# Kernel optimization log

Hardware: AMD Instinct MI355X
Metric: run time of the kernel (lower is better)

## Reference

```python
import jax, jax.numpy as jnp
import numpy as np

E, H = 300, 256          # embedding_dim, GRU hidden per direction
D = 2 * H                # BiGRU output / GCN feature dim
V, PAD = 30000, 0
B, T_LEN, C_LEN = 128, 50, 200
N_GCN = 2
OUT = 3


def _gru_dir(x, Wih, Whh, bih, bhh):
    # x: [B,S,E] -> [B,S,H]; torch GRU equations
    h0 = jnp.zeros((x.shape[0], Whh.shape[1]), x.dtype)
    def step(h, xt):
        gi = xt @ Wih.T + bih                 # [B,3H]
        gh = h @ Whh.T + bhh
        ir, iz, inn = jnp.split(gi, 3, axis=-1)
        hr, hz, hn = jnp.split(gh, 3, axis=-1)
        r = jax.nn.sigmoid(ir + hr)
        z = jax.nn.sigmoid(iz + hz)
        n = jnp.tanh(inn + r * hn)
        hnew = (1.0 - z) * n + z * h
        return hnew, hnew
    _, hs = jax.lax.scan(step, h0, jnp.swapaxes(x, 0, 1))
    return jnp.swapaxes(hs, 0, 1)


def _bigru(x, wih, whh, bih, bhh):
    # wih:[2,3H,E] whh:[2,3H,H] bih/bhh:[2,3H]
    f = _gru_dir(x, wih[0], whh[0], bih[0], bhh[0])
    b = _gru_dir(x[:, ::-1], wih[1], whh[1], bih[1], bhh[1])[:, ::-1]
    return jnp.concatenate([f, b], axis=-1)   # [B,S,2H]


def _stance_attn(tgt_emb, clm_emb, gt, gc):
    tgt_ht = _bigru(tgt_emb, *gt)
    clm_ht = _bigru(clm_emb, *gc)
    tgt_last = tgt_ht[:, -1]
    # 'dot' attention: weight[b,c] = claim_ht[b,c] . target_last_ht[b]
    w = jnp.einsum('bcd,bd->bc', clm_ht, tgt_last)
    # NOTE: original `weight.masked_fill(mask==0, -1e9)` result is DISCARDED
    # (non-inplace torch op), so the mask has no effect -> faithfully omitted.
    return tgt_ht, clm_ht, jax.nn.softmax(w, axis=1)


def _gcn(tgt_ht, clm_ht, Ws):
    # StanceGCN: cat nodes, N_GCN layers of dot-correlation attention + residual relu
    node = jnp.concatenate([tgt_ht, clm_ht], axis=1)   # [B,N,D]
    T = tgt_ht.shape[1]
    for i in range(Ws.shape[0]):
        # dot correlation reduces to pairwise inner products (no [B,N,N,D] blowup);
        # `corr_score.masked_fill(adj==0,...)` is also discarded in the source.
        corr = jax.nn.softmax(jnp.einsum('bid,bjd->bij', node, node), axis=2)
        trans = jnp.einsum('bnd,ed->bne', node, Ws[i])  # Linear(bias=False)
        node = jax.nn.relu(node + jnp.einsum('bij,bjd->bid', corr, trans))
    return node[:, :T], node[:, T:]


def setup_inputs() -> dict:
    key = jax.random.key(0)
    ks = iter(jax.random.split(key, 64))
    def norm(shape, s=0.05):
        return (jax.random.normal(next(ks), shape, jnp.float32) * s)
    d = {}
    d['task_id'] = 0
    d['task_target'] = jax.random.randint(next(ks), (B, T_LEN), 0, V)
    d['shared_target'] = jax.random.randint(next(ks), (B, T_LEN), 0, V)
    d['task_claim'] = jax.random.randint(next(ks), (B, C_LEN), 0, V)
    d['shared_claim'] = jax.random.randint(next(ks), (B, C_LEN), 0, V)
    d['task_mask'] = jax.random.randint(next(ks), (B, C_LEN), 0, 2).astype(jnp.int32)
    d['shared_mask'] = jax.random.randint(next(ks), (B, C_LEN), 0, 2).astype(jnp.int32)
    N = T_LEN + C_LEN
    d['task_adj'] = jax.random.randint(next(ks), (B, N, N), 0, 2).astype(jnp.int32)
    d['shared_adj'] = jax.random.randint(next(ks), (B, N, N), 0, 2).astype(jnp.int32)
    d['emb'] = norm((V, E), 0.1).at[PAD].set(0.0)
    for g in ['tgt', 'tgc', 'sgt', 'sgc']:
        d[g + '_wih'] = norm((2, 3 * H, E))
        d[g + '_whh'] = norm((2, 3 * H, H))
        d[g + '_bih'] = norm((2, 3 * H))
        d[g + '_bhh'] = norm((2, 3 * H))
    d['gcn_task_W'] = norm((N_GCN, D, D))
    d['gcn_shared_W'] = norm((N_GCN, D, D))
    d['lin_W'] = norm((OUT, 2 * D))
    d['lin_b'] = norm((OUT,))
    return d


def reference(task_id, task_target, shared_target, task_claim, shared_claim,
              task_mask, shared_mask, task_adj, shared_adj,
              emb,
              tgt_wih, tgt_whh, tgt_bih, tgt_bhh,
              tgc_wih, tgc_whh, tgc_bih, tgc_bhh,
              sgt_wih, sgt_whh, sgt_bih, sgt_bhh,
              sgc_wih, sgc_whh, sgc_bih, sgc_bhh,
              gcn_task_W, gcn_shared_W, lin_W, lin_b):
    # embedding lookups (eval mode: all dropouts are identity)
    tt, tc = emb[task_target], emb[task_claim]
    st, sc = emb[shared_target], emb[shared_claim]
    t_tgt, t_clm, t_w = _stance_attn(tt, tc,
                                     (tgt_wih, tgt_whh, tgt_bih, tgt_bhh),
                                     (tgc_wih, tgc_whh, tgc_bih, tgc_bhh))
    s_tgt, s_clm, s_w = _stance_attn(st, sc,
                                     (sgt_wih, sgt_whh, sgt_bih, sgt_bhh),
                                     (sgc_wih, sgc_whh, sgc_bih, sgc_bhh))
    _, t_clm_rep = _gcn(t_tgt, t_clm, gcn_task_W)
    _, s_clm_rep = _gcn(s_tgt, s_clm, gcn_shared_W)
    # StanceLinear: attention-weighted claim pooling, concat, final linear
    task_rep = jnp.einsum('bc,bcd->bd', t_w, t_clm_rep)
    shared_rep = jnp.einsum('bc,bcd->bd', s_w, s_clm_rep)
    final = jnp.concatenate([task_rep, shared_rep], axis=1)   # [B, 4H+4H]
    return final @ lin_W.T + lin_b                            # [B, 3]
```

## Files before the change

kernel.cpp:

```cpp
#include <hip/hip_runtime.h>
#include <hip/hip_bf16.h>

namespace {

constexpr int B_  = 128;
constexpr int TL  = 50, CL = 200, NNODE = 250;
constexpr int H_  = 256, D_ = 512;
constexpr long NODE_ELE = 128L * 250 * 512;

typedef __attribute__((ext_vector_type(8))) short bf16x8;
typedef __attribute__((ext_vector_type(4))) float f32x4;

__device__ inline float bits2f(unsigned v) { union { unsigned u; float f; } c; c.u = v; return c.f; }
__device__ inline unsigned f2bits(float x) { union { float f; unsigned u; } c; c.f = x; return c.u; }
__device__ inline unsigned short bfbits(float x) {
  __hip_bfloat16 b = __float2bfloat16(x);
  return *(unsigned short*)&b;
}
__device__ inline float bfsel(uint2 v, int r) {
  unsigned w = (r < 2) ? v.x : v.y;
  return bits2f((r & 1) ? (w & 0xFFFF0000u) : (w << 16));
}
__device__ inline float sigf(float x)  { return 1.f / (1.f + __expf(-x)); }
__device__ inline float tanhf_(float x){ return 1.f - 2.f / (__expf(2.f * x) + 1.f); }

struct BGemmArgs {
  const __hip_bfloat16* A; const __hip_bfloat16* B;
  const int* idx; const float* bias; const __hip_bfloat16* Res;
  void* C;
  long aStride, bStride, biasStride, cStride, rStride;
  int M, N, Kreal, lda, ldb, ldc, zShiftA;
};

template<bool GATHER, int OUT>
__global__ __launch_bounds__(256) void bgemm_k(BGemmArgs g) {
  __shared__ __align__(16) char As[2][16384];
  __shared__ __align__(16) char Bs[2][16384];
  const int z = blockIdx.z;
  const int m0 = blockIdx.x * 128, n0 = blockIdx.y * 128;
  const int tid = threadIdx.x;
  const int lane = tid & 63, wv = tid >> 6;
  const int wr = wv >> 1, wc = wv & 1;
  const __hip_bfloat16* Ab = GATHER ? g.A : g.A + (long)(z >> g.zShiftA) * g.aStride;
  const __hip_bfloat16* Bb = g.B + (long)z * g.bStride;

  long asrc[4], bsrc[4];
  int ldso[4];
  #pragma unroll
  for (int c2 = 0; c2 < 4; ++c2) {
    int o = c2 * 256 + tid;
    int row = o >> 3, ko = o & 7;
    int colel = 8 * (ko ^ (row & 7));
    long arow = GATHER ? (long)g.idx[m0 + row] * g.lda : (long)(m0 + row) * g.lda;
    asrc[c2] = arow + colel;
    bsrc[c2] = (long)(n0 + row) * g.ldb + colel;
    ldso[c2] = o * 16;
  }

  f32x4 acc[4][4];
  #pragma unroll
  for (int i = 0; i < 4; ++i)
    #pragma unroll
    for (int j = 0; j < 4; ++j) acc[i][j] = (f32x4){0.f, 0.f, 0.f, 0.f};

  const int KT = g.Kreal >> 6;
  #pragma unroll
  for (int c2 = 0; c2 < 4; ++c2) {
    __builtin_amdgcn_global_load_lds(
        (const __attribute__((address_space(1))) unsigned*)(Ab + asrc[c2]),
        (__attribute__((address_space(3))) unsigned*)(&As[0][0] + ldso[c2]), 16, 0, 0);
    __builtin_amdgcn_global_load_lds(
        (const __attribute__((address_space(1))) unsigned*)(Bb + bsrc[c2]),
        (__attribute__((address_space(3))) unsigned*)(&Bs[0][0] + ldso[c2]), 16, 0, 0);
  }
  __syncthreads();

  int buf = 0;
  for (int kt = 0; kt < KT; ++kt) {
    if (kt + 1 < KT) {
      long ko = (long)(kt + 1) * 64;
      #pragma unroll
      for (int c2 = 0; c2 < 4; ++c2) {
        __builtin_amdgcn_global_load_lds(
            (const __attribute__((address_space(1))) unsigned*)(Ab + asrc[c2] + ko),
            (__attribute__((address_space(3))) unsigned*)(&As[buf ^ 1][0] + ldso[c2]), 16, 0, 0);
        __builtin_amdgcn_global_load_lds(
            (const __attribute__((address_space(1))) unsigned*)(Bb + bsrc[c2] + ko),
            (__attribute__((address_space(3))) unsigned*)(&Bs[buf ^ 1][0] + ldso[c2]), 16, 0, 0);
      }
    }
    const char* ab = &As[buf][0];
    const char* bb = &Bs[buf][0];
    #pragma unroll
    for (int ks = 0; ks < 2; ++ks) {
      bf16x8 af[4], bfr[4];
      #pragma unroll
      for (int i = 0; i < 4; ++i) {
        int ra = wr * 64 + i * 16 + (lane & 15);
        af[i] = *(const bf16x8*)(ab + ((ra * 128 + ks * 64 + (lane >> 4) * 16) ^ ((ra & 7) << 4)));
        int rb = wc * 64 + i * 16 + (lane & 15);
        bfr[i] = *(const bf16x8*)(bb + ((rb * 128 + ks * 64 + (lane >> 4) * 16) ^ ((rb & 7) << 4)));
      }
      #pragma unroll
      for (int i = 0; i < 4; ++i)
        #pragma unroll
        for (int j = 0; j < 4; ++j)
          acc[i][j] = __builtin_amdgcn_mfma_f32_16x16x32_bf16(af[i], bfr[j], acc[i][j], 0, 0, 0);
    }
    __syncthreads();
    buf ^= 1;
  }

  const long cz = (long)z * g.cStride;
  #pragma unroll
  for (int i = 0; i < 4; ++i) {
    int rbase = m0 + wr * 64 + i * 16 + ((lane >> 4) << 2);
    #pragma unroll
    for (int j = 0; j < 4; ++j) {
      int col = n0 + wc * 64 + j * 16 + (lane & 15);
      #pragma unroll
      for (int r = 0; r < 4; ++r) {
        int row = rbase + r;
        float v = acc[i][j][r];
        if (OUT == 1) {
          if (row < g.M && col < g.N) {
            v += g.bias[(long)z * g.biasStride + col];
            ((__hip_bfloat16*)g.C)[cz + (long)row * g.ldc + col] = __float2bfloat16(v);
          }
        } else if (OUT == 3) {
          if (row < g.M)
            ((__hip_bfloat16*)g.C)[cz + (long)row * g.ldc + col] =
                __float2bfloat16(col < g.N ? v : 0.f);
        } else {
          if (row < g.M && col < g.N) {
            v += __bfloat162float(g.Res[(long)z * g.rStride + (long)row * g.ldc + col]);
            v = fmaxf(v, 0.f);
            ((__hip_bfloat16*)g.C)[cz + (long)row * g.ldc + col] = __float2bfloat16(v);
          }
        }
      }
    }
  }
}

struct CsmArgs { const __hip_bfloat16* in; __hip_bfloat16* outp; };

__global__ __launch_bounds__(256) void csm_k(CsmArgs g) {
  __shared__ __align__(16) char As[2][8192];
  __shared__ __align__(16) char Bs[2][32768];
  const int z = blockIdx.z;
  const int m0 = blockIdx.x * 64;
  const int tid = threadIdx.x;
  const int lane = tid & 63, wv = tid >> 6;
  const __hip_bfloat16* base = g.in + (long)z * 128000;

  long bsrc[8]; int bo[8];
  #pragma unroll
  for (int c2 = 0; c2 < 8; ++c2) {
    int o = c2 * 256 + tid;
    int row = o >> 3, ko = o & 7;
    bsrc[c2] = (long)row * 512 + 8 * (ko ^ (row & 7));
    bo[c2] = o * 16;
  }
  long asrc[2]; int ao[2];
  #pragma unroll
  for (int c2 = 0; c2 < 2; ++c2) {
    int o = c2 * 256 + tid;
    int row = o >> 3, ko = o & 7;
    asrc[c2] = (long)(m0 + row) * 512 + 8 * (ko ^ (row & 7));
    ao[c2] = o * 16;
  }

  f32x4 acc[16];
  #pragma unroll
  for (int j = 0; j < 16; ++j) acc[j] = (f32x4){0.f, 0.f, 0.f, 0.f};

  #pragma unroll
  for (int c2 = 0; c2 < 2; ++c2)
    __builtin_amdgcn_global_load_lds(
        (const __attribute__((address_space(1))) unsigned*)(base + asrc[c2]),
        (__attribute__((address_space(3))) unsigned*)(&As[0][0] + ao[c2]), 16, 0, 0);
  #pragma unroll
  for (int c2 = 0; c2 < 8; ++c2)
    __builtin_amdgcn_global_load_lds(
        (const __attribute__((address_space(1))) unsigned*)(base + bsrc[c2]),
        (__attribute__((address_space(3))) unsigned*)(&Bs[0][0] + bo[c2]), 16, 0, 0);
  __syncthreads();

  int buf = 0;
  for (int kt = 0; kt < 8; ++kt) {
    if (kt + 1 < 8) {
      long ko = (long)(kt + 1) * 64;
      #pragma unroll
      for (int c2 = 0; c2 < 2; ++c2)
        __builtin_amdgcn_global_load_lds(
            (const __attribute__((address_space(1))) unsigned*)(base + asrc[c2] + ko),
            (__attribute__((address_space(3))) unsigned*)(&As[buf ^ 1][0] + ao[c2]), 16, 0, 0);
      #pragma unroll
      for (int c2 = 0; c2 < 8; ++c2)
        __builtin_amdgcn_global_load_lds(
            (const __attribute__((address_space(1))) unsigned*)(base + bsrc[c2] + ko),
            (__attribute__((address_space(3))) unsigned*)(&Bs[buf ^ 1][0] + bo[c2]), 16, 0, 0);
    }
    const char* ab = &As[buf][0];
    const char* bb = &Bs[buf][0];
    #pragma unroll
    for (int ks = 0; ks < 2; ++ks) {
      int ra = wv * 16 + (lane & 15);
      bf16x8 af = *(const bf16x8*)(ab + ((ra * 128 + ks * 64 + (lane >> 4) * 16) ^ ((ra & 7) << 4)));
      #pragma unroll
      for (int j = 0; j < 16; ++j) {
        int rb = j * 16 + (lane & 15);
        bf16x8 bf = *(const bf16x8*)(bb + ((rb * 128 + ks * 64 + (lane >> 4) * 16) ^ ((rb & 7) << 4)));
        acc[j] = __builtin_amdgcn_mfma_f32_16x16x32_bf16(af, bf, acc[j], 0, 0, 0);
      }
    }
    __syncthreads();
    buf ^= 1;
  }

  const int c0 = lane & 15, rq = lane >> 4;
  const long obase = (long)z * 64000;
  #pragma unroll
  for (int r = 0; r < 4; ++r) {
    int row = m0 + wv * 16 + rq * 4 + r;
    float vals[16];
    float mx = -1e30f;
    #pragma unroll
    for (int j = 0; j < 16; ++j) {
      vals[j] = acc[j][r];
      if (j * 16 + c0 < 250) mx = fmaxf(mx, vals[j]);
    }
    #pragma unroll
    for (int o = 1; o < 16; o <<= 1) mx = fmaxf(mx, __shfl_xor(mx, o, 64));
    float s = 0.f;
    #pragma unroll
    for (int j = 0; j < 16; ++j) {
      float e = (j * 16 + c0 < 250) ? __expf(vals[j] - mx) : 0.f;
      vals[j] = e; s += e;
    }
    #pragma unroll
    for (int o = 1; o < 16; o <<= 1) s += __shfl_xor(s, o, 64);
    float inv = 1.f / s;
    if (row < 250) {
      #pragma unroll
      for (int j = 0; j < 16; ++j)
        g.outp[obase + (long)row * 256 + j * 16 + c0] = __float2bfloat16(vals[j] * inv);
    }
  }
}

struct PrepArgs {
  const float* whh[4];
  const float* gcnW[2];
  const float* emb;
  const float* wih[4];
  const float* bih[4];
  const float* bhh[4];
  __hip_bfloat16 *whhbf, *gcnWbf, *embbf;
  __hip_bfloat16* wihbf[4];
  float* biasC;
};

constexpr long PR0 = 1572864;
constexpr long PR1 = PR0 + 1048576;
constexpr long PR2 = PR1 + 9600000;
constexpr long PR3 = PR2 + 1966080;
constexpr long PR4 = PR3 + 6144;

__global__ __launch_bounds__(256) void prep_k(PrepArgs a) {
  long i = (long)blockIdx.x * 256 + threadIdx.x;
  if (i >= PR4) return;
  if (i < PR0) {
    int zz = (int)(i / 196608);
    long rem = i - (long)zz * 196608;
    a.whhbf[i] = __float2bfloat16(a.whh[zz >> 1][(long)(zz & 1) * 196608 + rem]);
  } else if (i < PR1) {
    long j = i - PR0;
    a.gcnWbf[j] = __float2bfloat16(a.gcnW[j / 524288][j % 524288]);
  } else if (i < PR2) {
    long j = i - PR1;
    long r = j / 320;
    int c = (int)(j - r * 320);
    a.embbf[j] = __float2bfloat16(c < 300 ? a.emb[r * 300 + c] : 0.f);
  } else if (i < PR3) {
    long j = i - PR2;
    int w = (int)(j / 491520);
    long k = j - (long)w * 491520;
    long r = k / 320;
    int c = (int)(k - r * 320);
    a.wihbf[w][k] = __float2bfloat16(c < 300 ? a.wih[w][r * 300 + c] : 0.f);
  } else {
    long j = i - PR3;
    int w = (int)(j / 1536);
    int k = (int)(j - (long)w * 1536);
    a.biasC[(long)w * 1536 + k] = a.bih[w][k] + ((k % 768) < 512 ? a.bhh[w][k] : 0.f);
  }
}

struct RecArgs {
  const __hip_bfloat16* whhbf;
  const __hip_bfloat16* gi[4];
  const float* bhh[4];
  __hip_bfloat16* nodebf;
};

__global__ __launch_bounds__(512, 2) void gru_rec_k(RecArgs a) {
  __shared__ __align__(16) char hbuf[2][8192];
  const int z = blockIdx.z;
  const int side = z >> 2, sq = (z >> 1) & 1, dir = z & 1;
  const int gidx = side * 2 + sq;
  const int T = sq ? CL : TL;
  const int toff = sq ? TL : 0;
  const __hip_bfloat16* gi = a.gi[gidx] + (long)dir * B_ * T * 768;
  const float* bhh = a.bhh[gidx] + dir * 768;
  const __hip_bfloat16* whh = a.whhbf + (long)z * 768 * 256;
  __hip_bfloat16* nodeb = a.nodebf + (long)side * NODE_ELE;
  const int b0 = blockIdx.x * 16;
  const int tid = threadIdx.x;
  const int lane = tid & 63, wv = tid >> 6;
  const int bcol = lane & 15, g4 = lane >> 4;
  const int u0 = wv * 32 + g4 * 4;
  const int swzh = (bcol & 15) << 4;

  bf16x8 Af[3][2][8];
  #pragma unroll
  for (int g = 0; g < 3; ++g)
    #pragma unroll
    for (int h = 0; h < 2; ++h)
      #pragma unroll
      for (int kt = 0; kt < 8; ++kt) {
        int row = g * 256 + wv * 32 + h * 16 + bcol;
        int col = kt * 32 + g4 * 8;
        Af[g][h][kt] = *(const bf16x8*)(whh + (long)row * 256 + col);
      }
  *(uint4*)&hbuf[0][tid * 16] = make_uint4(0, 0, 0, 0);
  const float4 bn0 = *(const float4*)&bhh[512 + u0];
  const float4 bn1 = *(const float4*)&bhh[512 + u0 + 16];
  __syncthreads();

  const __hip_bfloat16* gip = gi + ((long)(b0 + bcol) * T + (dir ? T - 1 : 0)) * 768 + u0;
  __hip_bfloat16* np = nodeb + ((long)(b0 + bcol) * NNODE + toff + (dir ? T - 1 : 0)) * D_
                       + dir * H_ + u0;
  const long gistep = dir ? -768L : 768L;
  const long nstep  = dir ? -(long)D_ : (long)D_;
  int cur = 0;

  float hreg[2][4];
  #pragma unroll
  for (int h = 0; h < 2; ++h)
    #pragma unroll
    for (int r = 0; r < 4; ++r) hreg[h][r] = 0.f;

  uint2 gv[3][2];
  #pragma unroll
  for (int g = 0; g < 3; ++g)
    #pragma unroll
    for (int h = 0; h < 2; ++h)
      gv[g][h] = *(const uint2*)(gip + g * 256 + h * 16);

  for (int t = 0; t < T; ++t) {
    const char* hib = &hbuf[cur][0];
    f32x4 c[3][2];
    #pragma unroll
    for (int g = 0; g < 3; ++g)
      #pragma unroll
      for (int h = 0; h < 2; ++h) c[g][h] = (f32x4){0.f, 0.f, 0.f, 0.f};
    const int rb = bcol * 512 + g4 * 16;
    #pragma unroll
    for (int kt = 0; kt < 8; ++kt) {
      bf16x8 bh = *(const bf16x8*)(hib + ((rb + kt * 64) ^ swzh));
      #pragma unroll
      for (int g = 0; g < 3; ++g)
        #pragma unroll
        for (int h = 0; h < 2; ++h)
          c[g][h] = __builtin_amdgcn_mfma_f32_16x16x32_bf16(Af[g][h][kt], bh, c[g][h], 0, 0, 0);
    }

    #pragma unroll
    for (int h = 0; h < 2; ++h) {
      float4 bn = h ? bn1 : bn0;
      #pragma unroll
      for (int r = 0; r < 4; ++r) {
        float bnv = (r == 0) ? bn.x : (r == 1) ? bn.y : (r == 2) ? bn.z : bn.w;
        float rr = sigf(bfsel(gv[0][h], r) + c[0][h][r]);
        float zz = sigf(bfsel(gv[1][h], r) + c[1][h][r]);
        float nn = tanhf_(bfsel(gv[2][h], r) + rr * (c[2][h][r] + bnv));
        hreg[h][r] = (1.f - zz) * nn + zz * hreg[h][r];
      }
    }

    {
      const __hip_bfloat16* gn = (t + 1 < T) ? gip + gistep : gip;
      gip = gn;
      #pragma unroll
      for (int g = 0; g < 3; ++g)
        #pragma unroll
        for (int h = 0; h < 2; ++h)
          gv[g][h] = *(const uint2*)(gn + g * 256 + h * 16);
    }

    const int ob0 = bcol * 512 + u0 * 2;
    char* hibn = &hbuf[cur ^ 1][0];
    #pragma unroll
    for (int h = 0; h < 2; ++h) {
      unsigned hb[4];
      #pragma unroll
      for (int r = 0; r < 4; ++r)
        hb[r] = (f2bits(hreg[h][r]) + 0x8000u) & 0xFFFF0000u;
      uint2 hiw;
      hiw.x = (hb[0] >> 16) | hb[1];
      hiw.y = (hb[2] >> 16) | hb[3];
      *(uint2*)(np + h * 16) = hiw;
      *(uint2*)(hibn + ((ob0 + h * 32) ^ swzh)) = hiw;
    }
    np += nstep;
    asm volatile("s_waitcnt lgkmcnt(0)" ::: "memory");
    __builtin_amdgcn_sched_barrier(0);
    __builtin_amdgcn_s_barrier();
    cur ^= 1;
  }
}

__global__ __launch_bounds__(256) void attn_k(const __hip_bfloat16* nodeAll,
                                              float* wT, float* wS) {
  int b = blockIdx.x, side = blockIdx.y;
  const __hip_bfloat16* node = nodeAll + (long)side * NODE_ELE;
  float* w = side ? wS : wT;
  __shared__ float tl[512];
  __shared__ float sc[CL];
  int tid = threadIdx.x;
  {
    const __hip_bfloat16* tr = node + ((long)b * NNODE + (TL - 1)) * D_;
    tl[tid]       = __bfloat162float(tr[tid]);
    tl[tid + 256] = __bfloat162float(tr[tid + 256]);
  }
  __syncthreads();
  int wid = tid >> 6, lane = tid & 63;
  for (int c = wid; c < CL; c += 4) {
    const __hip_bfloat16* row = node + ((long)b * NNODE + TL + c) * D_;
    uint4 v = *(const uint4*)(row + lane * 8);
    const float* tp = &tl[lane * 8];
    float acc = bits2f(v.x << 16)         * tp[0] + bits2f(v.x & 0xFFFF0000u) * tp[1]
              + bits2f(v.y << 16)         * tp[2] + bits2f(v.y & 0xFFFF0000u) * tp[3]
              + bits2f(v.z << 16)         * tp[4] + bits2f(v.z & 0xFFFF0000u) * tp[5]
              + bits2f(v.w << 16)         * tp[6] + bits2f(v.w & 0xFFFF0000u) * tp[7];
    #pragma unroll
    for (int o = 32; o; o >>= 1) acc += __shfl_xor(acc, o, 64);
    if (lane == 0) sc[c] = acc;
  }
  __syncthreads();
  if (wid == 0) {
    float v[4]; float m = -1e30f;
    #pragma unroll
    for (int i = 0; i < 4; ++i) {
      int c = lane + 64 * i;
      v[i] = (c < CL) ? sc[c] : -1e30f;
      m = fmaxf(m, v[i]);
    }
    #pragma unroll
    for (int o = 32; o; o >>= 1) m = fmaxf(m, __shfl_xor(m, o, 64));
    float s = 0.f;
    #pragma unroll
    for (int i = 0; i < 4; ++i) {
      int c = lane + 64 * i;
      v[i] = (c < CL) ? expf(v[i] - m) : 0.f;
      s += v[i];
    }
    #pragma unroll
    for (int o = 32; o; o >>= 1) s += __shfl_xor(s, o, 64);
    float inv = 1.f / s;
    #pragma unroll
    for (int i = 0; i < 4; ++i) {
      int c = lane + 64 * i;
      if (c < CL) w[(long)b * CL + c] = v[i] * inv;
    }
  }
}

__global__ __launch_bounds__(256) void rep_k(const __hip_bfloat16* nodeAll,
                                             const float* wT, const float* wS,
                                             float* rep) {
  int b = blockIdx.x, side = blockIdx.y;
  const __hip_bfloat16* node = nodeAll + (long)side * NODE_ELE;
  const float* w = side ? wS : wT;
  __shared__ float wl[CL];
  int tid = threadIdx.x;
  if (tid < CL) wl[tid] = w[(long)b * CL + tid];
  __syncthreads();
  #pragma unroll
  for (int h = 0; h < 2; ++h) {
    int d = tid + h * 256;
    float acc = 0.f;
    for (int c = 0; c < CL; ++c)
      acc = fmaf(wl[c], __bfloat162float(node[((long)b * NNODE + TL + c) * D_ + d]), acc);
    rep[((long)side * B_ + b) * D_ + d] = acc;
  }
}

__global__ __launch_bounds__(256) void final_k(const float* rep, const float* linW,
                                               const float* linb, float* out) {
  int b = blockIdx.x, tid = threadIdx.x;
  float a0 = 0.f, a1 = 0.f, a2 = 0.f;
  for (int d = tid; d < 1024; d += 256) {
    float x = rep[(long)(d >> 9) * (B_ * D_) + (long)b * D_ + (d & 511)];
    a0 = fmaf(x, linW[d], a0);
    a1 = fmaf(x, linW[1024 + d], a1);
    a2 = fmaf(x, linW[2048 + d], a2);
  }
  #pragma unroll
  for (int o = 32; o; o >>= 1) {
    a0 += __shfl_xor(a0, o, 64);
    a1 += __shfl_xor(a1, o, 64);
    a2 += __shfl_xor(a2, o, 64);
  }
  __shared__ float red[3][4];
  int wid = tid >> 6, lane = tid & 63;
  if (lane == 0) { red[0][wid] = a0; red[1][wid] = a1; red[2][wid] = a2; }
  __syncthreads();
  if (tid == 0) {
    out[b * 3 + 0] = red[0][0] + red[0][1] + red[0][2] + red[0][3] + linb[0];
    out[b * 3 + 1] = red[1][0] + red[1][1] + red[1][2] + red[1][3] + linb[1];
    out[b * 3 + 2] = red[2][0] + red[2][1] + red[2][2] + red[2][3] + linb[2];
  }
}

__global__ void diag_k(float* out, int n, float v) {
  int i = blockIdx.x * blockDim.x + threadIdx.x;
  if (i < n) out[i] = v;
}

}

extern "C" void kernel_launch(void* const* d_in, const int* in_sizes, int n_in,
                              void* d_out, int out_size, void* d_ws, size_t ws_size,
                              hipStream_t stream) {
  const int* task_target   = (const int*)d_in[1];
  const int* shared_target = (const int*)d_in[2];
  const int* task_claim    = (const int*)d_in[3];
  const int* shared_claim  = (const int*)d_in[4];
  const float* emb      = (const float*)d_in[9];
  const float* tgt_wih  = (const float*)d_in[10];
  const float* tgt_whh  = (const float*)d_in[11];
  const float* tgt_bih  = (const float*)d_in[12];
  const float* tgt_bhh  = (const float*)d_in[13];
  const float* tgc_wih  = (const float*)d_in[14];
  const float* tgc_whh  = (const float*)d_in[15];
  const float* tgc_bih  = (const float*)d_in[16];
  const float* tgc_bhh  = (const float*)d_in[17];
  const float* sgt_wih  = (const float*)d_in[18];
  const float* sgt_whh  = (const float*)d_in[19];
  const float* sgt_bih  = (const float*)d_in[20];
  const float* sgt_bhh  = (const float*)d_in[21];
  const float* sgc_wih  = (const float*)d_in[22];
  const float* sgc_whh  = (const float*)d_in[23];
  const float* sgc_bih  = (const float*)d_in[24];
  const float* sgc_bhh  = (const float*)d_in[25];
  const float* gcnW_task   = (const float*)d_in[26];
  const float* gcnW_shared = (const float*)d_in[27];
  const float* linW = (const float*)d_in[28];
  const float* linb = (const float*)d_in[29];
  float* out = (float*)d_out;

  const size_t SZ_WHH   = 3145728;
  const size_t SZ_GCNW  = 2097152;
  const size_t SZ_BIASC = 24576;
  const size_t SZ_ARENA = 196608000;
  const size_t SZ_NODE  = 65536000;
  const size_t SZ_W     = 102400;
  const size_t SZ_REP   = 524288;
  const size_t NEED = SZ_WHH + SZ_GCNW + SZ_BIASC + SZ_ARENA + SZ_NODE
                      + 2 * SZ_W + SZ_REP + 4096;

  if (ws_size < NEED) {
    diag_k<<<(out_size + 255) / 256, 256, 0, stream>>>(out, out_size,
                                                       (float)(ws_size >> 20));
    return;
  }

  char* p = (char*)d_ws;
  auto alloc = [&](size_t bytes) { char* r = p; p += (bytes + 255) & ~(size_t)255; return r; };
  __hip_bfloat16* whhbf  = (__hip_bfloat16*)alloc(SZ_WHH);
  __hip_bfloat16* gcnWbf = (__hip_bfloat16*)alloc(SZ_GCNW);
  float* biasC = (float*)alloc(SZ_BIASC);
  char* arena  = alloc(SZ_ARENA);
  char* nodeC  = alloc(SZ_NODE);
  float* wT    = (float*)alloc(SZ_W);
  float* wS    = (float*)alloc(SZ_W);
  float* rep   = (float*)alloc(SZ_REP);
  __hip_bfloat16* nodebf = (__hip_bfloat16*)nodeC;

  __hip_bfloat16* gi_tt = (__hip_bfloat16*)(arena);
  __hip_bfloat16* gi_tc = (__hip_bfloat16*)(arena + 19660800);
  __hip_bfloat16* gi_st = (__hip_bfloat16*)(arena + 98304000);
  __hip_bfloat16* gi_sc = (__hip_bfloat16*)(arena + 117964800);
  __hip_bfloat16* embbf = (__hip_bfloat16*)(nodeC);
  __hip_bfloat16* wihbf[4] = {
    (__hip_bfloat16*)(nodeC + 19200000),
    (__hip_bfloat16*)(nodeC + 20183040),
    (__hip_bfloat16*)(nodeC + 21166080),
    (__hip_bfloat16*)(nodeC + 22149120)};
  __hip_bfloat16* tmpbf  = (__hip_bfloat16*)(arena);
  __hip_bfloat16* corrbf = (__hip_bfloat16*)(arena + 65536000);
  __hip_bfloat16* transT = (__hip_bfloat16*)(arena + 98304000);

  {
    PrepArgs pa;
    pa.whh[0] = tgt_whh; pa.whh[1] = tgc_whh; pa.whh[2] = sgt_whh; pa.whh[3] = sgc_whh;
    pa.gcnW[0] = gcnW_task; pa.gcnW[1] = gcnW_shared;
    pa.emb = emb;
    pa.wih[0] = tgt_wih; pa.wih[1] = tgc_wih; pa.wih[2] = sgt_wih; pa.wih[3] = sgc_wih;
    pa.bih[0] = tgt_bih; pa.bih[1] = tgc_bih; pa.bih[2] = sgt_bih; pa.bih[3] = sgc_bih;
    pa.bhh[0] = tgt_bhh; pa.bhh[1] = tgc_bhh; pa.bhh[2] = sgt_bhh; pa.bhh[3] = sgc_bhh;
    pa.whhbf = whhbf; pa.gcnWbf = gcnWbf; pa.embbf = embbf;
    pa.wihbf[0] = wihbf[0]; pa.wihbf[1] = wihbf[1];
    pa.wihbf[2] = wihbf[2]; pa.wihbf[3] = wihbf[3];
    pa.biasC = biasC;
    prep_k<<<(int)((PR4 + 255) / 256), 256, 0, stream>>>(pa);
  }

  auto proj = [&](const int* idx, __hip_bfloat16* wih, const float* bias,
                  __hip_bfloat16* gi, int Mrows, int gx) {
    BGemmArgs ga{};
    ga.A = embbf; ga.idx = idx; ga.B = wih; ga.bias = bias; ga.C = gi;
    ga.aStride = 0; ga.bStride = 768L * 320; ga.biasStride = 768;
    ga.cStride = (long)Mrows * 768; ga.zShiftA = 0;
    ga.M = Mrows; ga.N = 768; ga.Kreal = 320; ga.lda = 320; ga.ldb = 320; ga.ldc = 768;
    bgemm_k<true, 1><<<dim3(gx, 6, 2), 256, 0, stream>>>(ga);
  };
  proj(task_target,   wihbf[0], biasC,        gi_tt, 6400, 50);
  proj(task_claim,    wihbf[1], biasC + 1536, gi_tc, 25600, 200);
  proj(shared_target, wihbf[2], biasC + 3072, gi_st, 6400, 50);
  proj(shared_claim,  wihbf[3], biasC + 4608, gi_sc, 25600, 200);

  RecArgs ra;
  ra.whhbf = whhbf;
  ra.gi[0] = gi_tt; ra.gi[1] = gi_tc; ra.gi[2] = gi_st; ra.gi[3] = gi_sc;
  ra.bhh[0] = tgt_bhh; ra.bhh[1] = tgc_bhh; ra.bhh[2] = sgt_bhh; ra.bhh[3] = sgc_bhh;
  ra.nodebf = nodebf;
  gru_rec_k<<<dim3(8, 1, 8), 512, 0, stream>>>(ra);

  attn_k<<<dim3(128, 2), 256, 0, stream>>>(nodebf, wT, wS);

  for (int layer = 0; layer < 2; ++layer) {
    const __hip_bfloat16* inbf = layer ? tmpbf : nodebf;
    CsmArgs cs{inbf, corrbf};
    csm_k<<<dim3(4, 1, 256), 256, 0, stream>>>(cs);
    BGemmArgs ta{};
    ta.A = gcnWbf + (long)layer * 262144; ta.B = inbf; ta.C = transT;
    ta.aStride = 524288; ta.bStride = 128000; ta.cStride = 131072; ta.zShiftA = 7;
    ta.M = 512; ta.N = 250; ta.Kreal = 512; ta.lda = 512; ta.ldb = 512; ta.ldc = 256;
    bgemm_k<false, 3><<<dim3(4, 2, 256), 256, 0, stream>>>(ta);
    BGemmArgs aa{};
    aa.A = corrbf; aa.B = transT; aa.Res = inbf;
    aa.C = layer ? (void*)nodebf : (void*)tmpbf;
    aa.aStride = 64000; aa.bStride = 131072; aa.cStride = 128000;
    aa.rStride = 128000; aa.zShiftA = 0;
    aa.M = 250; aa.N = 512; aa.Kreal = 256; aa.lda = 256; aa.ldb = 256; aa.ldc = 512;
    bgemm_k<false, 5><<<dim3(2, 4, 256), 256, 0, stream>>>(aa);
  }

  rep_k<<<dim3(128, 2), 256, 0, stream>>>(nodebf, wT, wS, rep);
  final_k<<<dim3(128), 256, 0, stream>>>(rep, linW, linb, out);
}
```

Measured before the change: 1.511 ms.

## Merge projection GEMMs into one launch and fuse GCN corr/trans/attn kernels

The four per-sequence input-projection GEMM launches become a single proj_k launch indexed by blockIdx.z, with out-of-range blocks exiting early. The correlation-softmax, transform GEMM and (on layer 0) attention-weight kernels are combined into one gfu_k launch that dispatches by block index and shares an 80KB LDS buffer. This cuts kernel launches and lets independent work fill the GPU together. The trade-off is that the larger shared LDS allocation may lower occupancy for the csm and trans parts.

Measured after the change: 1.367 ms. 1.11x faster.

```diff
diff --git a/kernel.cpp b/kernel.cpp
--- a/kernel.cpp
+++ b/kernel.cpp
@@ -23,16 +23,19 @@
 }
 __device__ inline float sigf(float x)  { return 1.f / (1.f + __expf(-x)); }
 __device__ inline float tanhf_(float x){ return 1.f - 2.f / (__expf(2.f * x) + 1.f); }
+__device__ inline void gld16(const __hip_bfloat16* src, char* dst) {
+  __builtin_amdgcn_global_load_lds(
+      (const __attribute__((address_space(1))) unsigned*)src,
+      (__attribute__((address_space(3))) unsigned*)dst, 16, 0, 0);
+}
 
 struct BGemmArgs {
-  const __hip_bfloat16* A; const __hip_bfloat16* B;
-  const int* idx; const float* bias; const __hip_bfloat16* Res;
+  const __hip_bfloat16* A; const __hip_bfloat16* B; const __hip_bfloat16* Res;
   void* C;
-  long aStride, bStride, biasStride, cStride, rStride;
-  int M, N, Kreal, lda, ldb, ldc, zShiftA;
+  long aStride, bStride, cStride, rStride;
+  int M, N, Kreal, lda, ldb, ldc;
 };
 
-template<bool GATHER, int OUT>
 __global__ __launch_bounds__(256) void bgemm_k(BGemmArgs g) {
   __shared__ __align__(16) char As[2][16384];
   __shared__ __align__(16) char Bs[2][16384];
@@ -41,7 +44,7 @@
   const int tid = threadIdx.x;
   const int lane = tid & 63, wv = tid >> 6;
   const int wr = wv >> 1, wc = wv & 1;
-  const __hip_bfloat16* Ab = GATHER ? g.A : g.A + (long)(z >> g.zShiftA) * g.aStride;
+  const __hip_bfloat16* Ab = g.A + (long)z * g.aStride;
   const __hip_bfloat16* Bb = g.B + (long)z * g.bStride;
 
   long asrc[4], bsrc[4];
@@ -51,8 +54,7 @@
     int o = c2 * 256 + tid;
     int row = o >> 3, ko = o & 7;
     int colel = 8 * (ko ^ (row & 7));
-    long arow = GATHER ? (long)g.idx[m0 + row] * g.lda : (long)(m0 + row) * g.lda;
-    asrc[c2] = arow + colel;
+    asrc[c2] = (long)(m0 + row) * g.lda + colel;
     bsrc[c2] = (long)(n0 + row) * g.ldb + colel;
     ldso[c2] = o * 16;
   }
@@ -66,12 +68,8 @@
   const int KT = g.Kreal >> 6;
   #pragma unroll
   for (int c2 = 0; c2 < 4; ++c2) {
-    __builtin_amdgcn_global_load_lds(
-        (const __attribute__((address_space(1))) unsigned*)(Ab + asrc[c2]),
-        (__attribute__((address_space(3))) unsigned*)(&As[0][0] + ldso[c2]), 16, 0, 0);
-    __builtin_amdgcn_global_load_lds(
-        (const __attribute__((address_space(1))) unsigned*)(Bb + bsrc[c2]),
-        (__attribute__((address_space(3))) unsigned*)(&Bs[0][0] + ldso[c2]), 16, 0, 0);
+    gld16(Ab + asrc[c2], &As[0][0] + ldso[c2]);
+    gld16(Bb + bsrc[c2], &Bs[0][0] + ldso[c2]);
   }
   __syncthreads();
 
@@ -81,12 +79,8 @@
       long ko = (long)(kt + 1) * 64;
       #pragma unroll
       for (int c2 = 0; c2 < 4; ++c2) {
-        __builtin_amdgcn_global_load_lds(
-            (const __attribute__((address_space(1))) unsigned*)(Ab + asrc[c2] + ko),
-            (__attribute__((address_space(3))) unsigned*)(&As[buf ^ 1][0] + ldso[c2]), 16, 0, 0);
-        __builtin_amdgcn_global_load_lds(
-            (const __attribute__((address_space(1))) unsigned*)(Bb + bsrc[c2] + ko),
-            (__attribute__((address_space(3))) unsigned*)(&Bs[buf ^ 1][0] + ldso[c2]), 16, 0, 0);
+        gld16(Ab + asrc[c2] + ko, &As[buf ^ 1][0] + ldso[c2]);
+        gld16(Bb + bsrc[c2] + ko, &Bs[buf ^ 1][0] + ldso[c2]);
       }
     }
     const char* ab = &As[buf][0];
@@ -121,38 +115,133 @@
       #pragma unroll
       for (int r = 0; r < 4; ++r) {
         int row = rbase + r;
-        float v = acc[i][j][r];
-        if (OUT == 1) {
-          if (row < g.M && col < g.N) {
-            v += g.bias[(long)z * g.biasStride + col];
-            ((__hip_bfloat16*)g.C)[cz + (long)row * g.ldc + col] = __float2bfloat16(v);
-          }
-        } else if (OUT == 3) {
-          if (row < g.M)
-            ((__hip_bfloat16*)g.C)[cz + (long)row * g.ldc + col] =
-                __float2bfloat16(col < g.N ? v : 0.f);
-        } else {
-          if (row < g.M && col < g.N) {
-            v += __bfloat162float(g.Res[(long)z * g.rStride + (long)row * g.ldc + col]);
-            v = fmaxf(v, 0.f);
-            ((__hip_bfloat16*)g.C)[cz + (long)row * g.ldc + col] = __float2bfloat16(v);
-          }
+        if (row < g.M && col < g.N) {
+          float v = acc[i][j][r];
+          v += __bfloat162float(g.Res[(long)z * g.rStride + (long)row * g.ldc + col]);
+          v = fmaxf(v, 0.f);
+          ((__hip_bfloat16*)g.C)[cz + (long)row * g.ldc + col] = __float2bfloat16(v);
         }
       }
     }
   }
 }
 
-struct CsmArgs { const __hip_bfloat16* in; __hip_bfloat16* outp; };
-
-__global__ __launch_bounds__(256) void csm_k(CsmArgs g) {
-  __shared__ __align__(16) char As[2][8192];
-  __shared__ __align__(16) char Bs[2][32768];
+struct ProjArgs {
+  const __hip_bfloat16* embbf;
+  const __hip_bfloat16* wih[4];
+  const int* tok[4];
+  const float* biasC;
+  __hip_bfloat16* gi[4];
+};
+
+__global__ __launch_bounds__(256) void proj_k(ProjArgs g) {
+  __shared__ __align__(16) char As[2][16384];
+  __shared__ __align__(16) char Bs[2][16384];
   const int z = blockIdx.z;
-  const int m0 = blockIdx.x * 64;
+  const int pj = z >> 1, dir = z & 1;
+  const int M = (pj & 1) ? 25600 : 6400;
+  const int m0 = blockIdx.x * 128;
+  if (m0 >= M) return;
+  const int n0 = blockIdx.y * 128;
   const int tid = threadIdx.x;
   const int lane = tid & 63, wv = tid >> 6;
-  const __hip_bfloat16* base = g.in + (long)z * 128000;
+  const int wr = wv >> 1, wc = wv & 1;
+  const __hip_bfloat16* Ab = g.embbf;
+  const __hip_bfloat16* Bb = g.wih[pj] + (long)dir * 768 * 320;
+  const int* idx = g.tok[pj];
+  const float* bias = g.biasC + pj * 1536 + dir * 768;
+  __hip_bfloat16* C = g.gi[pj] + (long)dir * M * 768;
+
+  long asrc[4], bsrc[4];
+  int ldso[4];
+  #pragma unroll
+  for (int c2 = 0; c2 < 4; ++c2) {
+    int o = c2 * 256 + tid;
+    int row = o >> 3, ko = o & 7;
+    int colel = 8 * (ko ^ (row & 7));
+    asrc[c2] = (long)idx[m0 + row] * 320 + colel;
+    bsrc[c2] = (long)(n0 + row) * 320 + colel;
+    ldso[c2] = o * 16;
+  }
+
+  f32x4 acc[4][4];
+  #pragma unroll
+  for (int i = 0; i < 4; ++i)
+    #pragma unroll
+    for (int j = 0; j < 4; ++j) acc[i][j] = (f32x4){0.f, 0.f, 0.f, 0.f};
+
+  #pragma unroll
+  for (int c2 = 0; c2 < 4; ++c2) {
+    gld16(Ab + asrc[c2], &As[0][0] + ldso[c2]);
+    gld16(Bb + bsrc[c2], &Bs[0][0] + ldso[c2]);
+  }
+  __syncthreads();
+
+  int buf = 0;
+  for (int kt = 0; kt < 5; ++kt) {
+    if (kt + 1 < 5) {
+      long ko = (long)(kt + 1) * 64;
+      #pragma unroll
+      for (int c2 = 0; c2 < 4; ++c2) {
+        gld16(Ab + asrc[c2] + ko, &As[buf ^ 1][0] + ldso[c2]);
+        gld16(Bb + bsrc[c2] + ko, &Bs[buf ^ 1][0] + ldso[c2]);
+      }
+    }
+    const char* ab = &As[buf][0];
+    const char* bb = &Bs[buf][0];
+    #pragma unroll
+    for (int ks = 0; ks < 2; ++ks) {
+      bf16x8 af[4], bfr[4];
+      #pragma unroll
+      for (int i = 0; i < 4; ++i) {
+        int ra = wr * 64 + i * 16 + (lane & 15);
+        af[i] = *(const bf16x8*)(ab + ((ra * 128 + ks * 64 + (lane >> 4) * 16) ^ ((ra & 7) << 4)));
+        int rb = wc * 64 + i * 16 + (lane & 15);
+        bfr[i] = *(const bf16x8*)(bb + ((rb * 128 + ks * 64 + (lane >> 4) * 16) ^ ((rb & 7) << 4)));
+      }
+      #pragma unroll
+      for (int i = 0; i < 4; ++i)
+        #pragma unroll
+        for (int j = 0; j < 4; ++j)
+          acc[i][j] = __builtin_amdgcn_mfma_f32_16x16x32_bf16(af[i], bfr[j], acc[i][j], 0, 0, 0);
+    }
+    __syncthreads();
+    buf ^= 1;
+  }
+
+  #pragma unroll
+  for (int i = 0; i < 4; ++i) {
+    int rbase = m0 + wr * 64 + i * 16 + ((lane >> 4) << 2);
+    #pragma unroll
+    for (int j = 0; j < 4; ++j) {
+      int col = n0 + wc * 64 + j * 16 + (lane & 15);
+      float bv = bias[col];
+      #pragma unroll
+      for (int r = 0; r < 4; ++r) {
+        int row = rbase + r;
+        C[(long)row * 768 + col] = __float2bfloat16(acc[i][j][r] + bv);
+      }
+    }
+  }
+}
+
+struct GfuArgs {
+  const __hip_bfloat16* inbf;
+  __hip_bfloat16* corrbf;
+  const __hip_bfloat16* gcnW;
+  __hip_bfloat16* transT;
+  const __hip_bfloat16* nodebf;
+  float *wT, *wS;
+};
+
+__device__ void csm_body(char* lds, const __hip_bfloat16* in, __hip_bfloat16* outp,
+                         int mblk, int z) {
+  char* As = lds;
+  char* Bs = lds + 16384;
+  const int m0 = mblk * 64;
+  const int tid = threadIdx.x;
+  const int lane = tid & 63, wv = tid >> 6;
+  const __hip_bfloat16* base = in + (long)z * 128000;
 
   long bsrc[8]; int bo[8];
   #pragma unroll
@@ -176,15 +265,9 @@
   for (int j = 0; j < 16; ++j) acc[j] = (f32x4){0.f, 0.f, 0.f, 0.f};
 
   #pragma unroll
-  for (int c2 = 0; c2 < 2; ++c2)
-    __builtin_amdgcn_global_load_lds(
-        (const __attribute__((address_space(1))) unsigned*)(base + asrc[c2]),
-        (__attribute__((address_space(3))) unsigned*)(&As[0][0] + ao[c2]), 16, 0, 0);
-  #pragma unroll
-  for (int c2 = 0; c2 < 8; ++c2)
-    __builtin_amdgcn_global_load_lds(
-        (const __attribute__((address_space(1))) unsigned*)(base + bsrc[c2]),
-        (__attribute__((address_space(3))) unsigned*)(&Bs[0][0] + bo[c2]), 16, 0, 0);
+  for (int c2 = 0; c2 < 2; ++c2) gld16(base + asrc[c2], As + ao[c2]);
+  #pragma unroll
+  for (int c2 = 0; c2 < 8; ++c2) gld16(base + bsrc[c2], Bs + bo[c2]);
   __syncthreads();
 
   int buf = 0;
@@ -192,18 +275,12 @@
     if (kt + 1 < 8) {
       long ko = (long)(kt + 1) * 64;
       #pragma unroll
-      for (int c2 = 0; c2 < 2; ++c2)
-        __builtin_amdgcn_global_load_lds(
-            (const __attribute__((address_space(1))) unsigned*)(base + asrc[c2] + ko),
-            (__attribute__((address_space(3))) unsigned*)(&As[buf ^ 1][0] + ao[c2]), 16, 0, 0);
-      #pragma unroll
-      for (int c2 = 0; c2 < 8; ++c2)
-        __builtin_amdgcn_global_load_lds(
-            (const __attribute__((address_space(1))) unsigned*)(base + bsrc[c2] + ko),
-            (__attribute__((address_space(3))) unsigned*)(&Bs[buf ^ 1][0] + bo[c2]), 16, 0, 0);
-    }
-    const char* ab = &As[buf][0];
-    const char* bb = &Bs[buf][0];
+      for (int c2 = 0; c2 < 2; ++c2) gld16(base + asrc[c2] + ko, As + (buf ^ 1) * 8192 + ao[c2]);
+      #pragma unroll
+      for (int c2 = 0; c2 < 8; ++c2) gld16(base + bsrc[c2] + ko, Bs + (buf ^ 1) * 32768 + bo[c2]);
+    }
+    const char* ab = As + buf * 8192;
+    const char* bb = Bs + buf * 32768;
     #pragma unroll
     for (int ks = 0; ks < 2; ++ks) {
       int ra = wv * 16 + (lane & 15);
@@ -245,8 +322,165 @@
     if (row < 250) {
       #pragma unroll
       for (int j = 0; j < 16; ++j)
-        g.outp[obase + (long)row * 256 + j * 16 + c0] = __float2bfloat16(vals[j] * inv);
-    }
+        outp[obase + (long)row * 256 + j * 16 + c0] = __float2bfloat16(vals[j] * inv);
+    }
+  }
+}
+
+__device__ void trans_body(char* lds, const __hip_bfloat16* W,
+                           const __hip_bfloat16* in, __hip_bfloat16* transT,
+                           int xb, int yb, int z) {
+  char* As = lds;
+  char* Bs = lds + 32768;
+  const int m0 = xb * 128, n0 = yb * 128;
+  const int tid = threadIdx.x;
+  const int lane = tid & 63, wv = tid >> 6;
+  const int wr = wv >> 1, wc = wv & 1;
+  const __hip_bfloat16* Ab = W + (long)(z >> 7) * 524288;
+  const __hip_bfloat16* Bb = in + (long)z * 128000;
+
+  long asrc[4], bsrc[4];
+  int ldso[4];
+  #pragma unroll
+  for (int c2 = 0; c2 < 4; ++c2) {
+    int o = c2 * 256 + tid;
+    int row = o >> 3, ko = o & 7;
+    int colel = 8 * (ko ^ (row & 7));
+    asrc[c2] = (long)(m0 + row) * 512 + colel;
+    bsrc[c2] = (long)(n0 + row) * 512 + colel;
+    ldso[c2] = o * 16;
+  }
+
+  f32x4 acc[4][4];
+  #pragma unroll
+  for (int i = 0; i < 4; ++i)
+    #pragma unroll
+    for (int j = 0; j < 4; ++j) acc[i][j] = (f32x4){0.f, 0.f, 0.f, 0.f};
+
+  #pragma unroll
+  for (int c2 = 0; c2 < 4; ++c2) {
+    gld16(Ab + asrc[c2], As + ldso[c2]);
+    gld16(Bb + bsrc[c2], Bs + ldso[c2]);
+  }
+  __syncthreads();
+
+  int buf = 0;
+  for (int kt = 0; kt < 8; ++kt) {
+    if (kt + 1 < 8) {
+      long ko = (long)(kt + 1) * 64;
+      #pragma unroll
+      for (int c2 = 0; c2 < 4; ++c2) {
+        gld16(Ab + asrc[c2] + ko, As + (buf ^ 1) * 16384 + ldso[c2]);
+        gld16(Bb + bsrc[c2] + ko, Bs + (buf ^ 1) * 16384 + ldso[c2]);
+      }
+    }
+    const char* ab = As + buf * 16384;
+    const char* bb = Bs + buf * 16384;
+    #pragma unroll
+    for (int ks = 0; ks < 2; ++ks) {
+      bf16x8 af[4], bfr[4];
+      #pragma unroll
+      for (int i = 0; i < 4; ++i) {
+        int ra = wr * 64 + i * 16 + (lane & 15);
+        af[i] = *(const bf16x8*)(ab + ((ra * 128 + ks * 64 + (lane >> 4) * 16) ^ ((ra & 7) << 4)));
+        int rb = wc * 64 + i * 16 + (lane & 15);
+        bfr[i] = *(const bf16x8*)(bb + ((rb * 128 + ks * 64 + (lane >> 4) * 16) ^ ((rb & 7) << 4)));
+      }
+      #pragma unroll
+      for (int i = 0; i < 4; ++i)
+        #pragma unroll
+        for (int j = 0; j < 4; ++j)
+          acc[i][j] = __builtin_amdgcn_mfma_f32_16x16x32_bf16(af[i], bfr[j], acc[i][j], 0, 0, 0);
+    }
+    __syncthreads();
+    buf ^= 1;
+  }
+
+  const long cz = (long)z * 131072;
+  #pragma unroll
+  for (int i = 0; i < 4; ++i) {
+    int rbase = m0 + wr * 64 + i * 16 + ((lane >> 4) << 2);
+    #pragma unroll
+    for (int j = 0; j < 4; ++j) {
+      int col = n0 + wc * 64 + j * 16 + (lane & 15);
+      if (col < 256) {
+        #pragma unroll
+        for (int r = 0; r < 4; ++r) {
+          int row = rbase + r;
+          transT[cz + (long)row * 256 + col] =
+              __float2bfloat16(col < 250 ? acc[i][j][r] : 0.f);
+        }
+      }
+    }
+  }
+}
+
+__device__ void attn_body(char* lds, const __hip_bfloat16* nodeAll,
+                          float* wT, float* wS, int b, int side) {
+  float* tl = (float*)lds;
+  float* sc = (float*)(lds + 2048);
+  const __hip_bfloat16* node = nodeAll + (long)side * NODE_ELE;
+  float* w = side ? wS : wT;
+  int tid = threadIdx.x;
+  {
+    const __hip_bfloat16* tr = node + ((long)b * NNODE + (TL - 1)) * D_;
+    tl[tid]       = __bfloat162float(tr[tid]);
+    tl[tid + 256] = __bfloat162float(tr[tid + 256]);
+  }
+  __syncthreads();
+  int wid = tid >> 6, lane = tid & 63;
+  for (int c = wid; c < CL; c += 4) {
+    const __hip_bfloat16* row = node + ((long)b * NNODE + TL + c) * D_;
+    uint4 v = *(const uint4*)(row + lane * 8);
+    const float* tp = &tl[lane * 8];
+    float acc = bits2f(v.x << 16)         * tp[0] + bits2f(v.x & 0xFFFF0000u) * tp[1]
+              + bits2f(v.y << 16)         * tp[2] + bits2f(v.y & 0xFFFF0000u) * tp[3]
+              + bits2f(v.z << 16)         * tp[4] + bits2f(v.z & 0xFFFF0000u) * tp[5]
+              + bits2f(v.w << 16)         * tp[6] + bits2f(v.w & 0xFFFF0000u) * tp[7];
+    #pragma unroll
+    for (int o = 32; o; o >>= 1) acc += __shfl_xor(acc, o, 64);
+    if (lane == 0) sc[c] = acc;
+  }
+  __syncthreads();
+  if (wid == 0) {
+    float v[4]; float m = -1e30f;
+    #pragma unroll
+    for (int i = 0; i < 4; ++i) {
+      int c = lane + 64 * i;
+      v[i] = (c < CL) ? sc[c] : -1e30f;
+      m = fmaxf(m, v[i]);
+    }
+    #pragma unroll
+    for (int o = 32; o; o >>= 1) m = fmaxf(m, __shfl_xor(m, o, 64));
+    float s = 0.f;
+    #pragma unroll
+    for (int i = 0; i < 4; ++i) {
+      int c = lane + 64 * i;
+      v[i] = (c < CL) ? expf(v[i] - m) : 0.f;
+      s += v[i];
+    }
+    #pragma unroll
+    for (int o = 32; o; o >>= 1) s += __shfl_xor(s, o, 64);
+    float inv = 1.f / s;
+    #pragma unroll
+    for (int i = 0; i < 4; ++i) {
+      int c = lane + 64 * i;
+      if (c < CL) w[(long)b * CL + c] = v[i] * inv;
+    }
+  }
+}
+
+__global__ __launch_bounds__(256) void gfu_k(GfuArgs g) {
+  __shared__ __align__(16) char lds[81920];
+  const int bid = blockIdx.x;
+  if (bid < 1024) {
+    csm_body(lds, g.inbf, g.corrbf, bid & 3, bid >> 2);
+  } else if (bid < 3072) {
+    int t = bid - 1024;
+    trans_body(lds, g.gcnW, g.inbf, g.transT, t & 3, (t >> 2) & 1, t >> 3);
+  } else {
+    int t = bid - 3072;
+    attn_body(lds, g.nodebf, g.wT, g.wS, t & 127, t >> 7);
   }
 }
 
@@ -419,62 +653,6 @@
     __builtin_amdgcn_sched_barrier(0);
     __builtin_amdgcn_s_barrier();
     cur ^= 1;
-  }
-}
-
-__global__ __launch_bounds__(256) void attn_k(const __hip_bfloat16* nodeAll,
-                                              float* wT, float* wS) {
-  int b = blockIdx.x, side = blockIdx.y;
-  const __hip_bfloat16* node = nodeAll + (long)side * NODE_ELE;
-  float* w = side ? wS : wT;
-  __shared__ float tl[512];
-  __shared__ float sc[CL];
-  int tid = threadIdx.x;
-  {
-    const __hip_bfloat16* tr = node + ((long)b * NNODE + (TL - 1)) * D_;
-    tl[tid]       = __bfloat162float(tr[tid]);
-    tl[tid + 256] = __bfloat162float(tr[tid + 256]);
-  }
-  __syncthreads();
-  int wid = tid >> 6, lane = tid & 63;
-  for (int c = wid; c < CL; c += 4) {
-    const __hip_bfloat16* row = node + ((long)b * NNODE + TL + c) * D_;
-    uint4 v = *(const uint4*)(row + lane * 8);
-    const float* tp = &tl[lane * 8];
-    float acc = bits2f(v.x << 16)         * tp[0] + bits2f(v.x & 0xFFFF0000u) * tp[1]
-              + bits2f(v.y << 16)         * tp[2] + bits2f(v.y & 0xFFFF0000u) * tp[3]
-              + bits2f(v.z << 16)         * tp[4] + bits2f(v.z & 0xFFFF0000u) * tp[5]
-              + bits2f(v.w << 16)         * tp[6] + bits2f(v.w & 0xFFFF0000u) * tp[7];
-    #pragma unroll
-    for (int o = 32; o; o >>= 1) acc += __shfl_xor(acc, o, 64);
-    if (lane == 0) sc[c] = acc;
-  }
-  __syncthreads();
-  if (wid == 0) {
-    float v[4]; float m = -1e30f;
-    #pragma unroll
-    for (int i = 0; i < 4; ++i) {
-      int c = lane + 64 * i;
-      v[i] = (c < CL) ? sc[c] : -1e30f;
-      m = fmaxf(m, v[i]);
-    }
-    #pragma unroll
-    for (int o = 32; o; o >>= 1) m = fmaxf(m, __shfl_xor(m, o, 64));
-    float s = 0.f;
-    #pragma unroll
-    for (int i = 0; i < 4; ++i) {
-      int c = lane + 64 * i;
-      v[i] = (c < CL) ? expf(v[i] - m) : 0.f;
-      s += v[i];
-    }
-    #pragma unroll
-    for (int o = 32; o; o >>= 1) s += __shfl_xor(s, o, 64);
-    float inv = 1.f / s;
-    #pragma unroll
-    for (int i = 0; i < 4; ++i) {
-      int c = lane + 64 * i;
-      if (c < CL) w[(long)b * CL + c] = v[i] * inv;
-    }
   }
 }
 
@@ -619,19 +797,16 @@
     prep_k<<<(int)((PR4 + 255) / 256), 256, 0, stream>>>(pa);
   }
 
-  auto proj = [&](const int* idx, __hip_bfloat16* wih, const float* bias,
-                  __hip_bfloat16* gi, int Mrows, int gx) {
-    BGemmArgs ga{};
-    ga.A = embbf; ga.idx = idx; ga.B = wih; ga.bias = bias; ga.C = gi;
-    ga.aStride = 0; ga.bStride = 768L * 320; ga.biasStride = 768;
-    ga.cStride = (long)Mrows * 768; ga.zShiftA = 0;
-    ga.M = Mrows; ga.N = 768; ga.Kreal = 320; ga.lda = 320; ga.ldb = 320; ga.ldc = 768;
-    bgemm_k<true, 1><<<dim3(gx, 6, 2), 256, 0, stream>>>(ga);
-  };
-  proj(task_target,   wihbf[0], biasC,        gi_tt, 6400, 50);
-  proj(task_claim,    wihbf[1], biasC + 1536, gi_tc, 25600, 200);
-  proj(shared_target, wihbf[2], biasC + 3072, gi_st, 6400, 50);
-  proj(shared_claim,  wihbf[3], biasC + 4608, gi_sc, 25600, 200);
+  {
+    ProjArgs ja;
+    ja.embbf = embbf;
+    ja.wih[0] = wihbf[0]; ja.wih[1] = wihbf[1]; ja.wih[2] = wihbf[2]; ja.wih[3] = wihbf[3];
+    ja.tok[0] = task_target; ja.tok[1] = task_claim;
+    ja.tok[2] = shared_target; ja.tok[3] = shared_claim;
+    ja.biasC = biasC;
+    ja.gi[0] = gi_tt; ja.gi[1] = gi_tc; ja.gi[2] = gi_st; ja.gi[3] = gi_sc;
+    proj_k<<<dim3(200, 6, 8), 256, 0, stream>>>(ja);
+  }
 
   RecArgs ra;
   ra.whhbf = whhbf;
@@ -640,24 +815,19 @@
   ra.nodebf = nodebf;
   gru_rec_k<<<dim3(8, 1, 8), 512, 0, stream>>>(ra);
 
-  attn_k<<<dim3(128, 2), 256, 0, stream>>>(nodebf, wT, wS);
-
   for (int layer = 0; layer < 2; ++layer) {
     const __hip_bfloat16* inbf = layer ? tmpbf : nodebf;
-    CsmArgs cs{inbf, corrbf};
-    csm_k<<<dim3(4, 1, 256), 256, 0, stream>>>(cs);
-    BGemmArgs ta{};
-    ta.A = gcnWbf + (long)layer * 262144; ta.B = inbf; ta.C = transT;
-    ta.aStride = 524288; ta.bStride = 128000; ta.cStride = 131072; ta.zShiftA = 7;
-    ta.M = 512; ta.N = 250; ta.Kreal = 512; ta.lda = 512; ta.ldb = 512; ta.ldc = 256;
-    bgemm_k<false, 3><<<dim3(4, 2, 256), 256, 0, stream>>>(ta);
+    GfuArgs gf;
+    gf.inbf = inbf; gf.corrbf = corrbf;
+    gf.gcnW = gcnWbf + (long)layer * 262144; gf.transT = transT;
+    gf.nodebf = nodebf; gf.wT = wT; gf.wS = wS;
+    gfu_k<<<dim3(layer == 0 ? 3328 : 3072), 256, 0, stream>>>(gf);
     BGemmArgs aa{};
     aa.A = corrbf; aa.B = transT; aa.Res = inbf;
     aa.C = layer ? (void*)nodebf : (void*)tmpbf;
-    aa.aStride = 64000; aa.bStride = 131072; aa.cStride = 128000;
-    aa.rStride = 128000; aa.zShiftA = 0;
+    aa.aStride = 64000; aa.bStride = 131072; aa.cStride = 128000; aa.rStride = 128000;
     aa.M = 250; aa.N = 512; aa.Kreal = 256; aa.lda = 256; aa.ldb = 256; aa.ldc = 512;
-    bgemm_k<false, 5><<<dim3(2, 4, 256), 256, 0, stream>>>(aa);
+    bgemm_k<<<dim3(2, 4, 256), 256, 0, stream>>>(aa);
   }
 
   rep_k<<<dim3(128, 2), 256, 0, stream>>>(nodebf, wT, wS, rep);
```
